# Performance work log

Hardware: AMD Instinct MI355X
Metric: run time of the kernel (lower is better)

Reference implementation:

```python
import jax, jax.numpy as jnp
import numpy as np

B, DX, DY = 128, 3, 3
D = DX * DY          # max_digit = 9
N = D * D            # num_nodes = 81
HID = 96
EMB = 16
ITERS = 4
M = B * N * D        # LSTM flattened rows = 93312


def _sudoku_adj():
    idx = np.arange(N)
    r, c = idx // D, idx % D
    br, bc = r // DX, c // DY
    same = (r[:, None] == r[None]) | (c[:, None] == c[None]) | ((br[:, None] == br[None]) & (bc[:, None] == bc[None]))
    return (same & ~np.eye(N, dtype=bool)).astype(np.float32)


def setup_inputs() -> dict:
    key = jax.random.key(0)
    ks = iter(jax.random.split(key, 40))

    def dense(shape, fan_in):
        return jax.random.normal(next(ks), shape, jnp.float32) / np.float32(np.sqrt(fan_in))

    return {
        "inputs": jax.random.randint(next(ks), (B, N), 0, D + 1, jnp.int32),
        "c0": jax.random.normal(next(ks), (M, HID), jnp.float32),
        "adj_cell": jnp.asarray((np.ones((D, D)) - np.eye(D)).astype(np.float32)),
        "adj_digit": jnp.asarray(_sudoku_adj()),
        "enc_W1": dense((3, EMB), 3), "enc_b1": jnp.zeros((EMB,), jnp.float32),
        "enc_W2": dense((EMB, HID), EMB), "enc_b2": jnp.zeros((HID,), jnp.float32),
        "cr_W": dense((3, HID, HID), HID), "cr_b": jnp.zeros((3, HID), jnp.float32),
        "dr_W": dense((3, HID, HID), HID), "dr_b": jnp.zeros((3, HID), jnp.float32),
        "gm_W1": dense((3 * HID, HID), 3 * HID), "gm_b1": jnp.zeros((HID,), jnp.float32),
        "gm_W2": dense((2, HID, HID), HID), "gm_b2": jnp.zeros((2, HID), jnp.float32),
        "lstm_Wih": dense((4 * HID, HID), HID), "lstm_Whh": dense((4 * HID, HID), HID),
        "lstm_bih": jnp.zeros((4 * HID,), jnp.float32), "lstm_bhh": jnp.zeros((4 * HID,), jnp.float32),
        "r_W12": dense((2, HID, HID), HID), "r_b12": jnp.zeros((2, HID), jnp.float32),
        "r_W3": dense((HID, 1), HID), "r_b3": jnp.zeros((1,), jnp.float32),
        "iters": ITERS,
    }


def _mlp(x, Ws, bs):
    # stacked MLP: ReLU between layers, none after the last
    L = Ws.shape[0]
    for l in range(L):
        x = x @ Ws[l] + bs[l]
        if l < L - 1:
            x = jax.nn.relu(x)
    return x


def _forward(inputs, c0, adj_cell, adj_digit, enc_W1, enc_b1, enc_W2, enc_b2,
             cr_W, cr_b, dr_W, dr_b, gm_W1, gm_b1, gm_W2, gm_b2,
             lstm_Wih, lstm_Whh, lstm_bih, lstm_bhh, r_W12, r_b12, r_W3, r_b3, iters):
    # mask: [B,N,D,3] = (blank, equals digit d+1, filled-with-other-digit)
    eq = inputs[:, :, None] == jnp.arange(1, D + 1, dtype=inputs.dtype)[None, None, :]
    given = inputs != 0
    mask = jnp.stack([
        jnp.broadcast_to((~given)[:, :, None], eq.shape), eq,
        (~eq) & given[:, :, None]
    ], axis=-1).astype(jnp.float32)

    X = jax.nn.relu(mask @ enc_W1 + enc_b1) @ enc_W2 + enc_b2  # [B,N,D,HID]

    def lstm_step(x, h, c):
        gates = x @ lstm_Wih.T + lstm_bih + h @ lstm_Whh.T + lstm_bhh
        i, f, g, o = jnp.split(gates, 4, axis=-1)  # PyTorch gate order i,f,g,o
        c = jax.nn.sigmoid(f) * c + jax.nn.sigmoid(i) * jnp.tanh(g)
        h = jax.nn.sigmoid(o) * jnp.tanh(c)
        return h, c

    def step(carry, _):
        h, c = carry  # [M,HID] each
        Hn = h.reshape(X.shape)
        # relational message passing: per-node MLP then sum over graph edges
        msg_cell = jnp.einsum('bndh,de->bneh', _mlp(Hn, cr_W, cr_b), adj_cell)
        msg_digit = jnp.einsum('bndh,nm->bmdh', _mlp(Hn, dr_W, dr_b), adj_digit)
        g = jnp.concatenate([X, msg_cell, msg_digit], axis=-1)  # [B,N,D,3*HID]
        g = jax.nn.relu(g @ gm_W1 + gm_b1)
        g = jax.nn.relu(g @ gm_W2[0] + gm_b2[0])
        g = g @ gm_W2[1] + gm_b2[1]
        h, c = lstm_step(g.reshape(-1, HID), h, c)
        Hn = h.reshape(X.shape)
        out = jax.nn.relu(Hn @ r_W12[0] + r_b12[0])
        out = jax.nn.relu(out @ r_W12[1] + r_b12[1])
        out = (out @ r_W3 + r_b3)[..., 0]  # [B,N,D]
        return (h, c), out

    (_, _), outs = jax.lax.scan(step, (X.reshape(-1, HID), c0), None, length=iters)
    return outs  # [iters,B,N,D]


def reference(inputs, c0, adj_cell, adj_digit, enc_W1, enc_b1, enc_W2, enc_b2,
              cr_W, cr_b, dr_W, dr_b, gm_W1, gm_b1, gm_W2, gm_b2,
              lstm_Wih, lstm_Whh, lstm_bih, lstm_bhh, r_W12, r_b12, r_W3, r_b3, iters):
    return _forward(inputs, c0, adj_cell, adj_digit, enc_W1, enc_b1, enc_W2, enc_b2,
                    cr_W, cr_b, dr_W, dr_b, gm_W1, gm_b1, gm_W2, gm_b2,
                    lstm_Wih, lstm_Whh, lstm_bih, lstm_bhh, r_W12, r_b12, r_W3, r_b3, iters)
```

## Files before the change

kernel.cpp:

```cpp
#include <hip/hip_runtime.h>
#include <hip/hip_bf16.h>

typedef unsigned short u16;
typedef __bf16 bf16x8 __attribute__((ext_vector_type(8)));
typedef float  f32x4  __attribute__((ext_vector_type(4)));
typedef u16    u16x8  __attribute__((ext_vector_type(8)));

#define HID   96
#define LDP   104
#define MROWS 93312
#define BN    10368
#define GRID_TILE 1458
#define LSTM_GRID 5832
#define SGS   104

#define FCH 9216

#define MFMA(a,b,c) __builtin_amdgcn_mfma_f32_16x16x32_bf16((a),(b),(c),0,0,0)

__device__ __forceinline__ float bf2f(u16 x){
  union { float f; unsigned u; } v; v.u = ((unsigned)x) << 16; return v.f;
}
__device__ __forceinline__ u16 f2bf(float f){
  union { float f; unsigned u; } v; v.f = f;
  unsigned r = v.u + 0x7fffu + ((v.u >> 16) & 1u);
  return (u16)(r >> 16);
}
__device__ __forceinline__ float frcp(float x){ return __builtin_amdgcn_rcpf(x); }
__device__ __forceinline__ float sigf(float x){ return frcp(1.f + __expf(-x)); }
__device__ __forceinline__ float tanhf_(float x){
  float xx = fminf(fmaxf(x, -15.f), 15.f);
  float e = __expf(-2.f * xx);
  return (1.f - e) * frcp(1.f + e);
}
__device__ __forceinline__ void lds_fence(){
  asm volatile("s_waitcnt lgkmcnt(0)" ::: "memory");
}

struct Frags { bf16x8 a0, a1, a2; };

__device__ __forceinline__ Frags load_afrags_g(const u16* __restrict__ A, size_t row0, int lane){
  int t16 = lane & 15, q = lane >> 4;
  const u16* p = A + (row0 + (size_t)t16) * 96 + q * 8;
  Frags f;
  f.a0 = *reinterpret_cast<const bf16x8*>(p);
  f.a1 = *reinterpret_cast<const bf16x8*>(p + 32);
  f.a2 = *reinterpret_cast<const bf16x8*>(p + 64);
  return f;
}
__device__ __forceinline__ Frags load_afrags_s(const u16* sA, int row0, int lane){
  int t16 = lane & 15, q = lane >> 4;
  const u16* p = sA + (row0 + t16) * LDP + q * 8;
  Frags f;
  f.a0 = *reinterpret_cast<const bf16x8*>(p);
  f.a1 = *reinterpret_cast<const bf16x8*>(p + 32);
  f.a2 = *reinterpret_cast<const bf16x8*>(p + 64);
  return f;
}

__device__ __forceinline__ void layer_g(Frags f, const u16* __restrict__ wb,
    const float* __restrict__ bias, u16* dst, int dstStride, size_t rowBase,
    bool relu, int lane)
{
  int t16 = lane & 15, q = lane >> 4;
  #pragma unroll
  for (int nt = 0; nt < 6; nt++){
    float b = bias ? bias[nt * 16 + t16] : 0.f;
    f32x4 acc = {b, b, b, b};
    const u16* wp = wb + nt * 1536 + lane * 8;
    acc = MFMA(f.a0, *reinterpret_cast<const bf16x8*>(wp),        acc);
    acc = MFMA(f.a1, *reinterpret_cast<const bf16x8*>(wp + 512),  acc);
    acc = MFMA(f.a2, *reinterpret_cast<const bf16x8*>(wp + 1024), acc);
    #pragma unroll
    for (int j = 0; j < 4; j++){
      float v = acc[j];
      if (relu) v = fmaxf(v, 0.f);
      dst[(rowBase + q * 4 + j) * (size_t)dstStride + nt * 16 + t16] = f2bf(v);
    }
  }
}

__device__ __forceinline__ void mfma6_g(f32x4* acc, int tbase, Frags f,
    const u16* __restrict__ wb, int lane)
{
  #pragma unroll
  for (int jt = 0; jt < 6; jt++){
    const u16* wp = wb + jt * 1536 + lane * 8;
    acc[tbase + jt] = MFMA(f.a0, *reinterpret_cast<const bf16x8*>(wp),        acc[tbase + jt]);
    acc[tbase + jt] = MFMA(f.a1, *reinterpret_cast<const bf16x8*>(wp + 512),  acc[tbase + jt]);
    acc[tbase + jt] = MFMA(f.a2, *reinterpret_cast<const bf16x8*>(wp + 1024), acc[tbase + jt]);
  }
}

__global__ __launch_bounds__(256) void k_prep2(const float* __restrict__ crW,
    const float* __restrict__ drW, const float* __restrict__ gmW1,
    const float* __restrict__ gmW2, const float* __restrict__ rW12,
    const float* __restrict__ Whh, u16* __restrict__ pWB)
{
  int b = blockIdx.x, tid = threadIdx.x;
  if (b < 12){
    u16* dst = pWB + b * FCH;
    const float* src;
    if (b < 3)       src = crW  + b * 9216;
    else if (b < 6)  src = drW  + (b - 3) * 9216;
    else if (b == 6) src = gmW1 + 9216;
    else if (b == 7) src = gmW1 + 18432;
    else if (b < 10) src = gmW2 + (b - 8) * 9216;
    else             src = rW12 + (b - 10) * 9216;
    #pragma unroll
    for (int i = 0; i < 36; i++){
      int idx = tid + i * 256;
      int f = idx >> 9, rem = idx & 511, l = rem >> 3, j = rem & 7;
      int nt = f / 3, kc = f - nt * 3;
      int n = nt * 16 + (l & 15);
      int k = ((l >> 4) << 3) + kc * 32 + j;
      dst[idx] = f2bf(src[k * 96 + n]);
    }
  } else {
    int bb = b - 12;
    u16* dst = pWB + (16 + bb) * FCH;
    const float* src = Whh + bb * 9216;
    #pragma unroll
    for (int i = 0; i < 36; i++){
      int idx = tid + i * 256;
      int f = idx >> 9, rem = idx & 511, l = rem >> 3, j = rem & 7;
      int nt = f / 3, kc = f - nt * 3;
      int n = nt * 16 + (l & 15);
      int k = ((l >> 4) << 3) + kc * 32 + j;
      dst[idx] = f2bf(src[n * 96 + k]);
    }
  }
}

__global__ __launch_bounds__(256) void k_prepf(const float* __restrict__ gmW2,
    const float* __restrict__ Wih, u16* __restrict__ pWB)
{
  __shared__ float sW[9216];
  int g = blockIdx.x, tid = threadIdx.x;
  for (int i = tid; i < 9216; i += 256) sW[i] = gmW2[9216 + i];
  __syncthreads();
  u16* dst = pWB + (12 + g) * FCH;
  #pragma unroll 2
  for (int i = 0; i < 36; i++){
    int idx = tid + i * 256;
    int f = idx >> 9, rem = idx & 511, l = rem >> 3, j = rem & 7;
    int nt = f / 3, kc = f - nt * 3;
    int n = nt * 16 + (l & 15);
    int k = ((l >> 4) << 3) + kc * 32 + j;
    const float* wr = Wih + (g * 96 + n) * 96;
    float acc = 0.f;
    for (int jj = 0; jj < 96; jj++) acc += sW[k * 96 + jj] * wr[jj];
    dst[idx] = f2bf(acc);
  }
}

__global__ void k_tables(const float* __restrict__ eW1, const float* __restrict__ eb1,
                         const float* __restrict__ eW2, const float* __restrict__ eb2,
                         const float* __restrict__ gmW1, const float* __restrict__ gmb1,
                         const float* __restrict__ bih, const float* __restrict__ bhh,
                         const float* __restrict__ gmb2, const float* __restrict__ Wih,
                         float* __restrict__ XTab, float* __restrict__ XgTab,
                         float* __restrict__ bsx)
{
  __shared__ float sX[3][96];
  int j = threadIdx.x;
  for (int n = j; n < 384; n += 128){
    float acc = bih[n] + bhh[n];
    const float* wr = Wih + n * 96;
    for (int jj = 0; jj < 96; jj++) acc += gmb2[96 + jj] * wr[jj];
    bsx[n] = acc;
  }
  if (j < 96){
    for (int ch = 0; ch < 3; ch++){
      float acc = eb2[j];
      for (int e = 0; e < 16; e++){
        float hv = fmaxf(eW1[ch * 16 + e] + eb1[e], 0.f);
        acc += hv * eW2[e * 96 + j];
      }
      sX[ch][j] = acc;
      XTab[ch * 96 + j] = acc;
    }
  }
  __syncthreads();
  if (j < 96){
    for (int ch = 0; ch < 3; ch++){
      float acc = gmb1[j];
      for (int k = 0; k < 96; k++) acc += sX[ch][k] * gmW1[k * 96 + j];
      XgTab[ch * 96 + j] = acc;
    }
  }
}

__global__ __launch_bounds__(256) void k_init(const int* __restrict__ inputs,
    const float* __restrict__ XTab, u16* __restrict__ h)
{
  int idx = blockIdx.x * 256 + threadIdx.x;
  int m = idx / 12, h8 = idx - m * 12;
  int bn = m / 9, d = m - bn * 9;
  int inp = inputs[bn];
  int ch = (inp == 0) ? 0 : ((inp == d + 1) ? 1 : 2);
  const float* xt = XTab + ch * 96 + h8 * 8;
  u16* hp = h + (size_t)m * 96 + h8 * 8;
  #pragma unroll
  for (int e = 0; e < 8; e++) hp[e] = f2bf(xt[e]);
}

__global__ __launch_bounds__(256) void k_ab3(const u16* __restrict__ h,
    u16* __restrict__ Y, u16* __restrict__ Z,
    const u16* __restrict__ pWB, const float* __restrict__ crB,
    const float* __restrict__ drB)
{
  __shared__ u16 sA[64 * LDP];
  const int tid = threadIdx.x, lane = tid & 63, wave = tid >> 6;
  const int wrow = wave * 16;
  const size_t rbase = (size_t)blockIdx.x * 64;

  Frags hf = load_afrags_g(h, rbase + wrow, lane);

  layer_g(hf, pWB, crB, sA, LDP, wrow, true, lane);                  lds_fence();
  Frags f = load_afrags_s(sA, wrow, lane);
  layer_g(f, pWB + 1 * FCH, crB + 96, sA, LDP, wrow, true, lane);    lds_fence();
  f = load_afrags_s(sA, wrow, lane);
  layer_g(f, pWB + 2 * FCH, crB + 192, sA, LDP, wrow, false, lane);  lds_fence();
  f = load_afrags_s(sA, wrow, lane);
  layer_g(f, pWB + 6 * FCH, nullptr, Y, 96, rbase + wrow, false, lane);
  lds_fence();

  layer_g(hf, pWB + 3 * FCH, drB, sA, LDP, wrow, true, lane);        lds_fence();
  f = load_afrags_s(sA, wrow, lane);
  layer_g(f, pWB + 4 * FCH, drB + 96, sA, LDP, wrow, true, lane);    lds_fence();
  f = load_afrags_s(sA, wrow, lane);
  layer_g(f, pWB + 5 * FCH, drB + 192, sA, LDP, wrow, false, lane);  lds_fence();
  f = load_afrags_s(sA, wrow, lane);
  layer_g(f, pWB + 7 * FCH, nullptr, Z, 96, rbase + wrow, false, lane);
}

__device__ __forceinline__ void addrow(float* s, const u16* p){
  u16x8 t = *reinterpret_cast<const u16x8*>(p);
  #pragma unroll
  for (int e = 0; e < 8; e++) s[e] += bf2f(t[e]);
}

__global__ __launch_bounds__(256) void k_msg(u16* __restrict__ Z,
    const u16* __restrict__ Y, u16* __restrict__ Ssum)
{
  __shared__ u16 sT[81 * LDP];
  const int tid = threadIdx.x;
  if (blockIdx.x >= 1152){
    int idx = (blockIdx.x - 1152) * 256 + tid;
    int bn = idx / 12, h8 = idx - bn * 12;
    const u16* base = Y + (size_t)bn * 864 + h8 * 8;
    float s[8];
    #pragma unroll
    for (int e = 0; e < 8; e++) s[e] = 0.f;
    #pragma unroll
    for (int d = 0; d < 9; d++){
      u16x8 v = *reinterpret_cast<const u16x8*>(base + d * 96);
      #pragma unroll
      for (int e = 0; e < 8; e++) s[e] += bf2f(v[e]);
    }
    u16x8 o;
    #pragma unroll
    for (int e = 0; e < 8; e++) o[e] = f2bf(s[e]);
    *reinterpret_cast<u16x8*>(Ssum + (size_t)bn * 96 + h8 * 8) = o;
    return;
  }
  const int b = blockIdx.x / 9, d = blockIdx.x - b * 9;
  const size_t base = ((size_t)b * 729 + d) * 96;
  for (int i = tid; i < 972; i += 256){
    int n = i / 12, k8 = i - n * 12;
    *reinterpret_cast<u16x8*>(sT + n * LDP + k8 * 8) =
      *reinterpret_cast<const u16x8*>(Z + base + (size_t)n * 864 + k8 * 8);
  }
  __syncthreads();
  for (int i = tid; i < 972; i += 256){
    int m = i / 12, k8 = i - m * 12;
    int r = m / 9, cc = m - r * 9;
    int br = (r / 3) * 3, bc = (cc / 3) * 3;
    float s[8];
    #pragma unroll
    for (int e = 0; e < 8; e++) s[e] = 0.f;
    #pragma unroll
    for (int c2 = 0; c2 < 9; c2++) if (c2 != cc) addrow(s, sT + (r * 9 + c2) * LDP + k8 * 8);
    #pragma unroll
    for (int r2 = 0; r2 < 9; r2++) if (r2 != r) addrow(s, sT + (r2 * 9 + cc) * LDP + k8 * 8);
    #pragma unroll
    for (int r2 = 0; r2 < 3; r2++)
      #pragma unroll
      for (int c2 = 0; c2 < 3; c2++){
        int rr = br + r2, c3 = bc + c2;
        if (rr != r && c3 != cc) addrow(s, sT + (rr * 9 + c3) * LDP + k8 * 8);
      }
    u16x8 o;
    #pragma unroll
    for (int e = 0; e < 8; e++) o[e] = f2bf(s[e]);
    *reinterpret_cast<u16x8*>(Z + base + (size_t)m * 864 + k8 * 8) = o;
  }
}

__global__ __launch_bounds__(256) void k_glr_a(u16* YG,
    const u16* __restrict__ Zd, const u16* __restrict__ Ssum,
    const int* __restrict__ inputs, const float* __restrict__ XgTab,
    const u16* __restrict__ pWB, const float* __restrict__ gmb2)
{
  __shared__ u16 sA[64 * LDP];
  const int tid = threadIdx.x, lane = tid & 63, wave = tid >> 6;
  const int wrow = wave * 16;
  const size_t rbase = (size_t)blockIdx.x * 64;

  for (int i = lane; i < 192; i += 64){
    int rl = i / 12, kc = i - rl * 12;
    int m = (int)rbase + wrow + rl;
    int bn = m / 9, d = m - bn * 9;
    int inp = inputs[bn];
    int ch = (inp == 0) ? 0 : ((inp == d + 1) ? 1 : 2);
    const float* xg = XgTab + ch * 96 + kc * 8;
    u16x8 vy = *reinterpret_cast<const u16x8*>(YG   + (size_t)m * 96 + kc * 8);
    u16x8 vz = *reinterpret_cast<const u16x8*>(Zd   + (size_t)m * 96 + kc * 8);
    u16x8 vs = *reinterpret_cast<const u16x8*>(Ssum + (size_t)bn * 96 + kc * 8);
    u16x8 o;
    #pragma unroll
    for (int e = 0; e < 8; e++)
      o[e] = f2bf(fmaxf(xg[e] + bf2f(vs[e]) - bf2f(vy[e]) + bf2f(vz[e]), 0.f));
    *reinterpret_cast<u16x8*>(sA + (wrow + rl) * LDP + kc * 8) = o;
  }
  lds_fence();

  Frags f = load_afrags_s(sA, wrow, lane);
  layer_g(f, pWB + 8 * FCH, gmb2, YG, 96, rbase + wrow, true, lane);
}

__global__ __launch_bounds__(256, 8) void k_lstm(const u16* __restrict__ A1,
    u16* h, const float* cin, float* cout,
    const float* __restrict__ bsx, const u16* __restrict__ pWB)
{
  __shared__ float sG[4][16][SGS];
  const int tid = threadIdx.x, lane = tid & 63, w = tid >> 6;
  const int t16 = lane & 15, q = lane >> 4;
  const size_t rbase = (size_t)blockIdx.x * 16;

  float cpre[6];
  #pragma unroll
  for (int e = 0; e < 6; e++){
    int idx = e * 256 + tid;
    int r = idx / 96, col = idx - r * 96;
    cpre[e] = cin[(rbase + r) * 96 + col];
  }

  f32x4 acc[6];
  #pragma unroll
  for (int nt = 0; nt < 6; nt++){
    float b = bsx[w * 96 + nt * 16 + t16];
    f32x4 a = {b, b, b, b};
    acc[nt] = a;
  }
  Frags aG = load_afrags_g(A1, rbase, lane);
  mfma6_g(acc, 0, aG, pWB + (12 + w) * FCH, lane);
  Frags ah = load_afrags_g(h, rbase, lane);
  mfma6_g(acc, 0, ah, pWB + (16 + w) * FCH, lane);

  #pragma unroll
  for (int nt = 0; nt < 6; nt++)
    #pragma unroll
    for (int j = 0; j < 4; j++)
      sG[w][q * 4 + j][nt * 16 + t16] = acc[nt][j];
  __syncthreads();

  #pragma unroll
  for (int e = 0; e < 6; e++){
    int idx = e * 256 + tid;
    int r = idx / 96, col = idx - r * 96;
    float iv = sG[0][r][col];
    float fv = sG[1][r][col];
    float gv = sG[2][r][col];
    float ov = sG[3][r][col];
    size_t m = rbase + r;
    float cn = sigf(fv) * cpre[e] + sigf(iv) * tanhf_(gv);
    float hn = sigf(ov) * tanhf_(cn);
    cout[m * 96 + col] = cn;
    h[m * 96 + col] = f2bf(hn);
  }
}

__global__ __launch_bounds__(256) void k_read(const u16* __restrict__ h,
    const u16* __restrict__ pWB, const float* __restrict__ rb12,
    const float* __restrict__ rW3, const float* __restrict__ rb3,
    float* __restrict__ out)
{
  __shared__ u16 sA[64 * LDP];
  const int tid = threadIdx.x, lane = tid & 63, wave = tid >> 6;
  const int wrow = wave * 16;
  const size_t rbase = (size_t)blockIdx.x * 64;

  Frags f = load_afrags_g(h, rbase + wrow, lane);
  layer_g(f, pWB + 10 * FCH, rb12, sA, LDP, wrow, true, lane);       lds_fence();
  f = load_afrags_s(sA, wrow, lane);
  layer_g(f, pWB + 11 * FCH, rb12 + 96, sA, LDP, wrow, true, lane);  lds_fence();

  int row = tid >> 2, part = tid & 3;
  float s = 0.f;
  const u16* rp = sA + row * LDP + part * 24;
  #pragma unroll
  for (int k = 0; k < 24; k++) s += bf2f(rp[k]) * rW3[part * 24 + k];
  s += __shfl_xor(s, 1);
  s += __shfl_xor(s, 2);
  if (part == 0) out[rbase + row] = s + rb3[0];
}

extern "C" void kernel_launch(void* const* d_in, const int* in_sizes, int n_in,
                              void* d_out, int out_size, void* d_ws, size_t ws_size,
                              hipStream_t stream)
{
  (void)in_sizes; (void)n_in; (void)out_size; (void)ws_size;
  const int*   inputs = (const int*)d_in[0];
  const float* c0     = (const float*)d_in[1];
  const float* eW1  = (const float*)d_in[4];
  const float* eb1  = (const float*)d_in[5];
  const float* eW2  = (const float*)d_in[6];
  const float* eb2  = (const float*)d_in[7];
  const float* crW  = (const float*)d_in[8];
  const float* crB  = (const float*)d_in[9];
  const float* drW  = (const float*)d_in[10];
  const float* drB  = (const float*)d_in[11];
  const float* gmW1 = (const float*)d_in[12];
  const float* gmb1 = (const float*)d_in[13];
  const float* gmW2 = (const float*)d_in[14];
  const float* gmb2 = (const float*)d_in[15];
  const float* Wih  = (const float*)d_in[16];
  const float* Whh  = (const float*)d_in[17];
  const float* bih  = (const float*)d_in[18];
  const float* bhh  = (const float*)d_in[19];
  const float* rW12 = (const float*)d_in[20];
  const float* rb12 = (const float*)d_in[21];
  const float* rW3  = (const float*)d_in[22];
  const float* rb3  = (const float*)d_in[23];

  char* ws = (char*)d_ws;
  float* XgTab = (float*)(ws);
  float* XTab  = (float*)(ws + 4096);
  float* bsx   = (float*)(ws + 6144);
  u16*   pWB   = (u16*)(ws + 8192);
  u16* h  = (u16*)(ws + 8192 + 401408);
  u16* B1 = h  + (size_t)MROWS * 96;
  u16* B2 = B1 + (size_t)MROWS * 96;
  float* c = (float*)(B2 + (size_t)MROWS * 96);
  u16* Ssum = (u16*)(c + (size_t)MROWS * 96);
  float* out = (float*)d_out;

  k_prep2<<<16, 256, 0, stream>>>(crW, drW, gmW1, gmW2, rW12, Whh, pWB);
  k_prepf<<<4, 256, 0, stream>>>(gmW2, Wih, pWB);
  k_tables<<<1, 128, 0, stream>>>(eW1, eb1, eW2, eb2, gmW1, gmb1, bih, bhh,
                                  gmb2, Wih, XTab, XgTab, bsx);
  k_init<<<(MROWS * 12) / 256, 256, 0, stream>>>(inputs, XTab, h);

  for (int it = 0; it < 4; ++it){
    const float* cin = (it == 0) ? c0 : c;
    k_ab3<<<GRID_TILE, 256, 0, stream>>>(h, B1, B2, pWB, crB, drB);
    k_msg<<<1152 + 486, 256, 0, stream>>>(B2, B1, Ssum);
    k_glr_a<<<GRID_TILE, 256, 0, stream>>>(B1, B2, Ssum, inputs, XgTab, pWB, gmb2);
    k_lstm<<<LSTM_GRID, 256, 0, stream>>>(B1, h, cin, c, bsx, pWB);
    k_read<<<GRID_TILE, 256, 0, stream>>>(h, pWB, rb12, rW3, rb3,
                                          out + (size_t)it * MROWS);
  }
}
```

Measured before the change: 716.0 us.

## Fuse gate MLP, LSTM and readout kernels; fold last MLP layers into gmW1 slices

Merges the gate-MLP layer, the LSTM step and the readout MLP into one kernel that keeps the 64-row tile in LDS. This removes the B1 round trip and the h re-read between the three former kernels. The third cr/dr MLP layer is also pre-multiplied with the matching gmW1 slice (weights and bias folded on device), cutting two GEMMs per iteration in k_ab3. Weight-prep kernels are split across more blocks with padded LDS. Risks include lower occupancy from the larger LDS footprint in the fused kernel, serialized row-group loops, and extra bf16 rounding from the folded weights.

```diff
diff --git a/kernel.cpp b/kernel.cpp
--- a/kernel.cpp
+++ b/kernel.cpp
@@ -11,8 +11,8 @@
 #define MROWS 93312
 #define BN    10368
 #define GRID_TILE 1458
-#define LSTM_GRID 5832
 #define SGS   104
+#define PST   97
 
 #define FCH 9216
 
@@ -80,33 +80,34 @@
   }
 }
 
-__device__ __forceinline__ void mfma6_g(f32x4* acc, int tbase, Frags f,
+__device__ __forceinline__ void mfma6_g(f32x4* acc, Frags f,
     const u16* __restrict__ wb, int lane)
 {
   #pragma unroll
   for (int jt = 0; jt < 6; jt++){
     const u16* wp = wb + jt * 1536 + lane * 8;
-    acc[tbase + jt] = MFMA(f.a0, *reinterpret_cast<const bf16x8*>(wp),        acc[tbase + jt]);
-    acc[tbase + jt] = MFMA(f.a1, *reinterpret_cast<const bf16x8*>(wp + 512),  acc[tbase + jt]);
-    acc[tbase + jt] = MFMA(f.a2, *reinterpret_cast<const bf16x8*>(wp + 1024), acc[tbase + jt]);
+    acc[jt] = MFMA(f.a0, *reinterpret_cast<const bf16x8*>(wp),        acc[jt]);
+    acc[jt] = MFMA(f.a1, *reinterpret_cast<const bf16x8*>(wp + 512),  acc[jt]);
+    acc[jt] = MFMA(f.a2, *reinterpret_cast<const bf16x8*>(wp + 1024), acc[jt]);
   }
 }
 
 __global__ __launch_bounds__(256) void k_prep2(const float* __restrict__ crW,
-    const float* __restrict__ drW, const float* __restrict__ gmW1,
-    const float* __restrict__ gmW2, const float* __restrict__ rW12,
-    const float* __restrict__ Whh, u16* __restrict__ pWB)
+    const float* __restrict__ drW, const float* __restrict__ gmW2,
+    const float* __restrict__ rW12, const float* __restrict__ Whh,
+    u16* __restrict__ pWB)
 {
   int b = blockIdx.x, tid = threadIdx.x;
-  if (b < 12){
-    u16* dst = pWB + b * FCH;
-    const float* src;
-    if (b < 3)       src = crW  + b * 9216;
-    else if (b < 6)  src = drW  + (b - 3) * 9216;
-    else if (b == 6) src = gmW1 + 9216;
-    else if (b == 7) src = gmW1 + 18432;
-    else if (b < 10) src = gmW2 + (b - 8) * 9216;
-    else             src = rW12 + (b - 10) * 9216;
+  if (b < 7){
+    const float* src; int ch;
+    if      (b == 0){ src = crW;          ch = 0;  }
+    else if (b == 1){ src = crW  + 9216;  ch = 1;  }
+    else if (b == 2){ src = drW;          ch = 3;  }
+    else if (b == 3){ src = drW  + 9216;  ch = 4;  }
+    else if (b == 4){ src = gmW2;         ch = 8;  }
+    else if (b == 5){ src = rW12;         ch = 10; }
+    else            { src = rW12 + 9216;  ch = 11; }
+    u16* dst = pWB + ch * FCH;
     #pragma unroll
     for (int i = 0; i < 36; i++){
       int idx = tid + i * 256;
@@ -117,7 +118,7 @@
       dst[idx] = f2bf(src[k * 96 + n]);
     }
   } else {
-    int bb = b - 12;
+    int bb = b - 7;
     u16* dst = pWB + (16 + bb) * FCH;
     const float* src = Whh + bb * 9216;
     #pragma unroll
@@ -132,25 +133,69 @@
   }
 }
 
+__global__ __launch_bounds__(256) void k_prepc(const float* __restrict__ crW,
+    const float* __restrict__ crB, const float* __restrict__ drW,
+    const float* __restrict__ drB, const float* __restrict__ gmW1,
+    u16* __restrict__ pWB, float* __restrict__ bY, float* __restrict__ bZ)
+{
+  __shared__ float sM[96 * PST];
+  __shared__ float sW[96 * PST];
+  int b = blockIdx.x, g = b / 9, seg = b - g * 9, tid = threadIdx.x;
+  const float* L = (g == 0 ? crW : drW) + 2 * 9216;
+  const float* R = gmW1 + (g == 0 ? 9216 : 18432);
+  for (int i = tid; i < 9216; i += 256){
+    int r = i / 96, cc = i - r * 96;
+    sM[r * PST + cc] = L[i];
+    sW[r * PST + cc] = R[i];
+  }
+  __syncthreads();
+  if (seg == 0){
+    const float* bv = (g == 0 ? crB : drB) + 192;
+    float* bo = (g == 0 ? bY : bZ);
+    for (int n = tid; n < 96; n += 256){
+      float a = 0.f;
+      for (int j = 0; j < 96; j++) a += bv[j] * sW[j * PST + n];
+      bo[n] = a;
+    }
+  }
+  u16* dst = pWB + (g == 0 ? 2 : 5) * FCH;
+  #pragma unroll
+  for (int i = 0; i < 4; i++){
+    int idx = seg * 1024 + tid + i * 256;
+    int f = idx >> 9, rem = idx & 511, l = rem >> 3, j = rem & 7;
+    int nt = f / 3, kc = f - nt * 3;
+    int n = nt * 16 + (l & 15);
+    int k = ((l >> 4) << 3) + kc * 32 + j;
+    float a = 0.f;
+    #pragma unroll 4
+    for (int jj = 0; jj < 96; jj++) a += sM[k * PST + jj] * sW[jj * PST + n];
+    dst[idx] = f2bf(a);
+  }
+}
+
 __global__ __launch_bounds__(256) void k_prepf(const float* __restrict__ gmW2,
     const float* __restrict__ Wih, u16* __restrict__ pWB)
 {
-  __shared__ float sW[9216];
-  int g = blockIdx.x, tid = threadIdx.x;
-  for (int i = tid; i < 9216; i += 256) sW[i] = gmW2[9216 + i];
+  __shared__ float sW[96 * PST];
+  int b = blockIdx.x, g = b / 9, seg = b - g * 9, tid = threadIdx.x;
+  for (int i = tid; i < 9216; i += 256){
+    int r = i / 96, cc = i - r * 96;
+    sW[r * PST + cc] = gmW2[9216 + i];
+  }
   __syncthreads();
   u16* dst = pWB + (12 + g) * FCH;
-  #pragma unroll 2
-  for (int i = 0; i < 36; i++){
-    int idx = tid + i * 256;
+  #pragma unroll
+  for (int i = 0; i < 4; i++){
+    int idx = seg * 1024 + tid + i * 256;
     int f = idx >> 9, rem = idx & 511, l = rem >> 3, j = rem & 7;
     int nt = f / 3, kc = f - nt * 3;
     int n = nt * 16 + (l & 15);
     int k = ((l >> 4) << 3) + kc * 32 + j;
     const float* wr = Wih + (g * 96 + n) * 96;
-    float acc = 0.f;
-    for (int jj = 0; jj < 96; jj++) acc += sW[k * 96 + jj] * wr[jj];
-    dst[idx] = f2bf(acc);
+    float a = 0.f;
+    #pragma unroll 4
+    for (int jj = 0; jj < 96; jj++) a += sW[k * PST + jj] * wr[jj];
+    dst[idx] = f2bf(a);
   }
 }
 
@@ -208,7 +253,8 @@
 __global__ __launch_bounds__(256) void k_ab3(const u16* __restrict__ h,
     u16* __restrict__ Y, u16* __restrict__ Z,
     const u16* __restrict__ pWB, const float* __restrict__ crB,
-    const float* __restrict__ drB)
+    const float* __restrict__ drB, const float* __restrict__ bY,
+    const float* __restrict__ bZ)
 {
   __shared__ u16 sA[64 * LDP];
   const int tid = threadIdx.x, lane = tid & 63, wave = tid >> 6;
@@ -221,18 +267,14 @@
   Frags f = load_afrags_s(sA, wrow, lane);
   layer_g(f, pWB + 1 * FCH, crB + 96, sA, LDP, wrow, true, lane);    lds_fence();
   f = load_afrags_s(sA, wrow, lane);
-  layer_g(f, pWB + 2 * FCH, crB + 192, sA, LDP, wrow, false, lane);  lds_fence();
-  f = load_afrags_s(sA, wrow, lane);
-  layer_g(f, pWB + 6 * FCH, nullptr, Y, 96, rbase + wrow, false, lane);
+  layer_g(f, pWB + 2 * FCH, bY, Y, 96, rbase + wrow, false, lane);
   lds_fence();
 
   layer_g(hf, pWB + 3 * FCH, drB, sA, LDP, wrow, true, lane);        lds_fence();
   f = load_afrags_s(sA, wrow, lane);
   layer_g(f, pWB + 4 * FCH, drB + 96, sA, LDP, wrow, true, lane);    lds_fence();
   f = load_afrags_s(sA, wrow, lane);
-  layer_g(f, pWB + 5 * FCH, drB + 192, sA, LDP, wrow, false, lane);  lds_fence();
-  f = load_afrags_s(sA, wrow, lane);
-  layer_g(f, pWB + 7 * FCH, nullptr, Z, 96, rbase + wrow, false, lane);
+  layer_g(f, pWB + 5 * FCH, bZ, Z, 96, rbase + wrow, false, lane);
 }
 
 __device__ __forceinline__ void addrow(float* s, const u16* p){
@@ -298,14 +340,20 @@
   }
 }
 
-__global__ __launch_bounds__(256) void k_glr_a(u16* YG,
+__global__ __launch_bounds__(256) void k_fuse(const u16* __restrict__ Y,
     const u16* __restrict__ Zd, const u16* __restrict__ Ssum,
     const int* __restrict__ inputs, const float* __restrict__ XgTab,
-    const u16* __restrict__ pWB, const float* __restrict__ gmb2)
+    const u16* __restrict__ pWB, const float* __restrict__ gmb2,
+    u16* h, const float* cin, float* cout,
+    const float* __restrict__ bsx, const float* __restrict__ rb12,
+    const float* __restrict__ rW3, const float* __restrict__ rb3,
+    float* __restrict__ out)
 {
   __shared__ u16 sA[64 * LDP];
-  const int tid = threadIdx.x, lane = tid & 63, wave = tid >> 6;
-  const int wrow = wave * 16;
+  __shared__ float sG[4][16][SGS];
+  const int tid = threadIdx.x, lane = tid & 63, w = tid >> 6;
+  const int t16 = lane & 15, q = lane >> 4;
+  const int wrow = w * 16;
   const size_t rbase = (size_t)blockIdx.x * 64;
 
   for (int i = lane; i < 192; i += 64){
@@ -315,7 +363,7 @@
     int inp = inputs[bn];
     int ch = (inp == 0) ? 0 : ((inp == d + 1) ? 1 : 2);
     const float* xg = XgTab + ch * 96 + kc * 8;
-    u16x8 vy = *reinterpret_cast<const u16x8*>(YG   + (size_t)m * 96 + kc * 8);
+    u16x8 vy = *reinterpret_cast<const u16x8*>(Y    + (size_t)m * 96 + kc * 8);
     u16x8 vz = *reinterpret_cast<const u16x8*>(Zd   + (size_t)m * 96 + kc * 8);
     u16x8 vs = *reinterpret_cast<const u16x8*>(Ssum + (size_t)bn * 96 + kc * 8);
     u16x8 o;
@@ -325,81 +373,69 @@
     *reinterpret_cast<u16x8*>(sA + (wrow + rl) * LDP + kc * 8) = o;
   }
   lds_fence();
-
+  {
+    Frags f = load_afrags_s(sA, wrow, lane);
+    layer_g(f, pWB + 8 * FCH, gmb2, sA, LDP, wrow, true, lane);
+  }
+  __syncthreads();
+
+  float bias6[6];
+  #pragma unroll
+  for (int nt = 0; nt < 6; nt++) bias6[nt] = bsx[w * 96 + nt * 16 + t16];
+
+  for (int rg = 0; rg < 4; rg++){
+    float cpre[6];
+    #pragma unroll
+    for (int e = 0; e < 6; e++){
+      int idx = e * 256 + tid;
+      int r = idx / 96, col = idx - r * 96;
+      cpre[e] = cin[(rbase + rg * 16 + r) * 96 + col];
+    }
+    Frags fh = load_afrags_g(h, rbase + rg * 16, lane);
+    Frags fa = load_afrags_s(sA, rg * 16, lane);
+    f32x4 acc[6];
+    #pragma unroll
+    for (int nt = 0; nt < 6; nt++){
+      f32x4 a = {bias6[nt], bias6[nt], bias6[nt], bias6[nt]};
+      acc[nt] = a;
+    }
+    mfma6_g(acc, fa, pWB + (12 + w) * FCH, lane);
+    mfma6_g(acc, fh, pWB + (16 + w) * FCH, lane);
+    #pragma unroll
+    for (int nt = 0; nt < 6; nt++)
+      #pragma unroll
+      for (int j = 0; j < 4; j++)
+        sG[w][q * 4 + j][nt * 16 + t16] = acc[nt][j];
+    __syncthreads();
+
+    #pragma unroll
+    for (int e = 0; e < 6; e++){
+      int idx = e * 256 + tid;
+      int r = idx / 96, col = idx - r * 96;
+      float iv = sG[0][r][col];
+      float fv = sG[1][r][col];
+      float gv = sG[2][r][col];
+      float ov = sG[3][r][col];
+      size_t m = rbase + rg * 16 + r;
+      float cn = sigf(fv) * cpre[e] + sigf(iv) * tanhf_(gv);
+      float hn = sigf(ov) * tanhf_(cn);
+      cout[m * 96 + col] = cn;
+      u16 hb = f2bf(hn);
+      h[m * 96 + col] = hb;
+      sA[(rg * 16 + r) * LDP + col] = hb;
+    }
+    __syncthreads();
+  }
+
+  u16* sS = (u16*)sG;
   Frags f = load_afrags_s(sA, wrow, lane);
-  layer_g(f, pWB + 8 * FCH, gmb2, YG, 96, rbase + wrow, true, lane);
-}
-
-__global__ __launch_bounds__(256, 8) void k_lstm(const u16* __restrict__ A1,
-    u16* h, const float* cin, float* cout,
-    const float* __restrict__ bsx, const u16* __restrict__ pWB)
-{
-  __shared__ float sG[4][16][SGS];
-  const int tid = threadIdx.x, lane = tid & 63, w = tid >> 6;
-  const int t16 = lane & 15, q = lane >> 4;
-  const size_t rbase = (size_t)blockIdx.x * 16;
-
-  float cpre[6];
-  #pragma unroll
-  for (int e = 0; e < 6; e++){
-    int idx = e * 256 + tid;
-    int r = idx / 96, col = idx - r * 96;
-    cpre[e] = cin[(rbase + r) * 96 + col];
-  }
-
-  f32x4 acc[6];
-  #pragma unroll
-  for (int nt = 0; nt < 6; nt++){
-    float b = bsx[w * 96 + nt * 16 + t16];
-    f32x4 a = {b, b, b, b};
-    acc[nt] = a;
-  }
-  Frags aG = load_afrags_g(A1, rbase, lane);
-  mfma6_g(acc, 0, aG, pWB + (12 + w) * FCH, lane);
-  Frags ah = load_afrags_g(h, rbase, lane);
-  mfma6_g(acc, 0, ah, pWB + (16 + w) * FCH, lane);
-
-  #pragma unroll
-  for (int nt = 0; nt < 6; nt++)
-    #pragma unroll
-    for (int j = 0; j < 4; j++)
-      sG[w][q * 4 + j][nt * 16 + t16] = acc[nt][j];
-  __syncthreads();
-
-  #pragma unroll
-  for (int e = 0; e < 6; e++){
-    int idx = e * 256 + tid;
-    int r = idx / 96, col = idx - r * 96;
-    float iv = sG[0][r][col];
-    float fv = sG[1][r][col];
-    float gv = sG[2][r][col];
-    float ov = sG[3][r][col];
-    size_t m = rbase + r;
-    float cn = sigf(fv) * cpre[e] + sigf(iv) * tanhf_(gv);
-    float hn = sigf(ov) * tanhf_(cn);
-    cout[m * 96 + col] = cn;
-    h[m * 96 + col] = f2bf(hn);
-  }
-}
-
-__global__ __launch_bounds__(256) void k_read(const u16* __restrict__ h,
-    const u16* __restrict__ pWB, const float* __restrict__ rb12,
-    const float* __restrict__ rW3, const float* __restrict__ rb3,
-    float* __restrict__ out)
-{
-  __shared__ u16 sA[64 * LDP];
-  const int tid = threadIdx.x, lane = tid & 63, wave = tid >> 6;
-  const int wrow = wave * 16;
-  const size_t rbase = (size_t)blockIdx.x * 64;
-
-  Frags f = load_afrags_g(h, rbase + wrow, lane);
-  layer_g(f, pWB + 10 * FCH, rb12, sA, LDP, wrow, true, lane);       lds_fence();
-  f = load_afrags_s(sA, wrow, lane);
-  layer_g(f, pWB + 11 * FCH, rb12 + 96, sA, LDP, wrow, true, lane);  lds_fence();
+  layer_g(f, pWB + 10 * FCH, rb12, sS, LDP, wrow, true, lane);       lds_fence();
+  f = load_afrags_s(sS, wrow, lane);
+  layer_g(f, pWB + 11 * FCH, rb12 + 96, sS, LDP, wrow, true, lane);  lds_fence();
 
   int row = tid >> 2, part = tid & 3;
   float s = 0.f;
-  const u16* rp = sA + row * LDP + part * 24;
+  const u16* rp = sS + row * LDP + part * 24;
   #pragma unroll
   for (int k = 0; k < 24; k++) s += bf2f(rp[k]) * rW3[part * 24 + k];
   s += __shfl_xor(s, 1);
@@ -439,27 +475,29 @@
   float* XgTab = (float*)(ws);
   float* XTab  = (float*)(ws + 4096);
   float* bsx   = (float*)(ws + 6144);
-  u16*   pWB   = (u16*)(ws + 8192);
-  u16* h  = (u16*)(ws + 8192 + 401408);
+  float* bY    = (float*)(ws + 7680);
+  float* bZ    = (float*)(ws + 8064);
+  u16*   pWB   = (u16*)(ws + 8704);
+  u16* h  = (u16*)(ws + 409600);
   u16* B1 = h  + (size_t)MROWS * 96;
   u16* B2 = B1 + (size_t)MROWS * 96;
   float* c = (float*)(B2 + (size_t)MROWS * 96);
   u16* Ssum = (u16*)(c + (size_t)MROWS * 96);
   float* out = (float*)d_out;
 
-  k_prep2<<<16, 256, 0, stream>>>(crW, drW, gmW1, gmW2, rW12, Whh, pWB);
-  k_prepf<<<4, 256, 0, stream>>>(gmW2, Wih, pWB);
+  k_prep2<<<11, 256, 0, stream>>>(crW, drW, gmW2, rW12, Whh, pWB);
+  k_prepc<<<18, 256, 0, stream>>>(crW, crB, drW, drB, gmW1, pWB, bY, bZ);
+  k_prepf<<<36, 256, 0, stream>>>(gmW2, Wih, pWB);
   k_tables<<<1, 128, 0, stream>>>(eW1, eb1, eW2, eb2, gmW1, gmb1, bih, bhh,
                                   gmb2, Wih, XTab, XgTab, bsx);
   k_init<<<(MROWS * 12) / 256, 256, 0, stream>>>(inputs, XTab, h);
 
   for (int it = 0; it < 4; ++it){
     const float* cin = (it == 0) ? c0 : c;
-    k_ab3<<<GRID_TILE, 256, 0, stream>>>(h, B1, B2, pWB, crB, drB);
+    k_ab3<<<GRID_TILE, 256, 0, stream>>>(h, B1, B2, pWB, crB, drB, bY, bZ);
     k_msg<<<1152 + 486, 256, 0, stream>>>(B2, B1, Ssum);
-    k_glr_a<<<GRID_TILE, 256, 0, stream>>>(B1, B2, Ssum, inputs, XgTab, pWB, gmb2);
-    k_lstm<<<LSTM_GRID, 256, 0, stream>>>(B1, h, cin, c, bsx, pWB);
-    k_read<<<GRID_TILE, 256, 0, stream>>>(h, pWB, rb12, rW3, rb3,
+    k_fuse<<<GRID_TILE, 256, 0, stream>>>(B1, B2, Ssum, inputs, XgTab, pWB, gmb2,
+                                          h, cin, c, bsx, rb12, rW3, rb3,
                                           out + (size_t)it * MROWS);
   }
 }
```

Result: slower. 819.2 us (+14.4%).
